# Optimization experiments

Measured on AMD Instinct MI355X. Metric: run time of the kernel, lower is better.

The kernel has to match this reference:

```python
import jax, jax.numpy as jnp
import numpy as np

B, T, D = 2, 2048, 2048
H, KV = 32, 8
HD = D // H            # 64
N_REP = H // KV        # 4


def setup_inputs() -> dict:
    key = jax.random.key(0)
    ks = jax.random.split(key, 5)
    x = jax.random.normal(ks[0], (B, T, D), dtype=jnp.float32)
    # RoPE frequencies: angle[t, i] = t / 10000^(2i/HD), i in [0, HD/2)
    inv_freq = 1.0 / (10000.0 ** (jnp.arange(0, HD, 2, dtype=jnp.float32) / HD))
    ang = jnp.arange(T, dtype=jnp.float32)[:, None] * inv_freq[None, :]  # [T, HD/2]
    freqs_cos = jnp.cos(ang)
    freqs_sin = jnp.sin(ang)
    # causal additive mask [1,1,T,T]
    r = jnp.arange(T)
    mask = jnp.where(r[None, :] > r[:, None], -1e9, 0.0).astype(jnp.float32)[None, None]
    s = 0.02
    wq = jax.random.normal(ks[1], (D, H * HD), dtype=jnp.float32) * s
    wk = jax.random.normal(ks[2], (D, KV * HD), dtype=jnp.float32) * s
    wv = jax.random.normal(ks[3], (D, KV * HD), dtype=jnp.float32) * s
    wo = jax.random.normal(ks[4], (H * HD, D), dtype=jnp.float32) * s
    return {"x": x, "freqs_cos": freqs_cos, "freqs_sin": freqs_sin, "mask": mask,
            "wq": wq, "wk": wk, "wv": wv, "wo": wo}


def _rope(t, cos, sin):
    # t: [B, T, h, HD]; complex rotation on consecutive (even, odd) pairs
    t2 = t.reshape(*t.shape[:-1], HD // 2, 2)
    c = cos[None, :, None, :]
    s = sin[None, :, None, :]
    o0 = t2[..., 0] * c - t2[..., 1] * s
    o1 = t2[..., 0] * s + t2[..., 1] * c
    return jnp.stack([o0, o1], axis=-1).reshape(t.shape)


def reference(x, freqs_cos, freqs_sin, mask, wq, wk, wv, wo):
    q = (x @ wq).reshape(B, T, H, HD)
    k = (x @ wk).reshape(B, T, KV, HD)
    v = (x @ wv).reshape(B, T, KV, HD)
    q = _rope(q, freqs_cos, freqs_sin)
    k = _rope(k, freqs_cos, freqs_sin)
    # GQA expand: each kv head repeated N_REP times consecutively
    k = jnp.repeat(k, N_REP, axis=2)  # [B, T, H, HD]
    v = jnp.repeat(v, N_REP, axis=2)
    scores = jnp.einsum('bqhd,bkhd->bhqk', q, k) / jnp.sqrt(jnp.float32(HD))
    scores = scores + mask
    attn = jax.nn.softmax(scores, axis=-1)
    out = jnp.einsum('bhqk,bkhd->bqhd', attn, v).reshape(B, T, H * HD)
    return out @ wo
```

## Files before the change

### kernel.cpp

```cpp
#include <hip/hip_runtime.h>
#include <hip/hip_bf16.h>

#define T_SEQ 2048
#define NROWS 4096
#define QKS   2560

typedef __attribute__((ext_vector_type(8))) short short8;
typedef __attribute__((ext_vector_type(4))) float f32x4;
typedef __attribute__((ext_vector_type(16))) float f32x16;
typedef __attribute__((ext_vector_type(2))) int i32x2;
typedef __attribute__((ext_vector_type(2))) unsigned int u32x2;

#define KC 0.18033688f

__device__ __forceinline__ unsigned short f2bf(float f) {
    unsigned u = __builtin_bit_cast(unsigned, f);
    u += 0x7FFF + ((u >> 16) & 1);
    return (unsigned short)(u >> 16);
}
__device__ __forceinline__ float bf2f(unsigned short s) {
    unsigned u = ((unsigned)s) << 16;
    return __builtin_bit_cast(float, u);
}

__device__ __forceinline__ void gload_lds16(const void* g, void* l) {
    __builtin_amdgcn_global_load_lds(
        (const __attribute__((address_space(1))) unsigned int*)g,
        (__attribute__((address_space(3))) unsigned int*)l,
        16, 0, 0);
}

__device__ __forceinline__ f32x4 mfma16(short8 a, short8 b, f32x4 c) {
    return __builtin_amdgcn_mfma_f32_16x16x32_bf16(a, b, c, 0, 0, 0);
}
__device__ __forceinline__ f32x16 mfma32(short8 a, short8 b, f32x16 c) {
    return __builtin_amdgcn_mfma_f32_32x32x16_bf16(a, b, c, 0, 0, 0);
}

__device__ __forceinline__ unsigned cvtpk_bf16(float lo, float hi) {
    unsigned r;
    asm("v_cvt_pk_bf16_f32 %0, %1, %2" : "=v"(r) : "v"(lo), "v"(hi));
    return r;
}

__device__ __forceinline__ short8 frag_from_u32(unsigned w0, unsigned w1, unsigned w2, unsigned w3) {
    union { unsigned u[4]; short8 s; } t;
    t.u[0] = w0; t.u[1] = w1; t.u[2] = w2; t.u[3] = w3;
    return t.s;
}

__global__ __launch_bounds__(256) void prep(const float* __restrict__ x,
                                            const float* __restrict__ wq,
                                            const float* __restrict__ wk,
                                            const float* __restrict__ wv,
                                            short* __restrict__ xb,
                                            short* __restrict__ wT) {
    __shared__ float tile[32][33];
    const int bid = blockIdx.x, t = threadIdx.x;
    if (bid < 4096) {
        const int i = bid * 256 + t;
        const float4 a = ((const float4*)x)[i * 2];
        const float4 b = ((const float4*)x)[i * 2 + 1];
        ((short8*)xb)[i] = frag_from_u32(cvtpk_bf16(a.x, a.y), cvtpk_bf16(a.z, a.w),
                                         cvtpk_bf16(b.x, b.y), cvtpk_bf16(b.z, b.w));
        return;
    }
    const int r = bid - 4096;
    const int bx = r % 96, by = r / 96;
    const float* S; int srcN, nt, dstRow0;
    if (bx < 64)      { S = wq; srcN = 2048; nt = bx;      dstRow0 = 0;    }
    else if (bx < 80) { S = wk; srcN = 512;  nt = bx - 64; dstRow0 = 2048; }
    else              { S = wv; srcN = 512;  nt = bx - 80; dstRow0 = 2560; }
    const int n0 = nt * 32, k0 = by * 32;
#pragma unroll
    for (int j = 0; j < 4; ++j) {
        int lin = t + 256 * j;
        int kk = lin >> 5, nn = lin & 31;
        tile[kk][nn] = S[(size_t)(k0 + kk) * srcN + n0 + nn];
    }
    __syncthreads();
#pragma unroll
    for (int j = 0; j < 4; ++j) {
        int lin = t + 256 * j;
        int nn = lin >> 5, kk = lin & 31;
        wT[(size_t)(dstRow0 + n0 + nn) * 2048 + k0 + kk] = (short)f2bf(tile[kk][nn]);
    }
}

__global__ __launch_bounds__(256) void transpose_f32_bf16(const float* __restrict__ S,
                                                          short* __restrict__ D,
                                                          int K, int N) {
    __shared__ float tile[32][33];
    const int n0 = blockIdx.x * 32, k0 = blockIdx.y * 32;
    const int t = threadIdx.x;
#pragma unroll
    for (int j = 0; j < 4; ++j) {
        int lin = t + 256 * j;
        int kk = lin >> 5, nn = lin & 31;
        tile[kk][nn] = S[(size_t)(k0 + kk) * N + n0 + nn];
    }
    __syncthreads();
#pragma unroll
    for (int j = 0; j < 4; ++j) {
        int lin = t + 256 * j;
        int nn = lin >> 5, kk = lin & 31;
        D[(size_t)(n0 + nn) * K + k0 + kk] = (short)f2bf(tile[kk][nn]);
    }
}

__global__ __launch_bounds__(256) void rope_vt(unsigned short* __restrict__ qk,
                                               const float* __restrict__ cosp,
                                               const float* __restrict__ sinp,
                                               const short* __restrict__ vbuf,
                                               short* __restrict__ vt) {
    __shared__ short tile[32][33];
    const int bid = blockIdx.x, t = threadIdx.x;
    if (bid < 2048) {
        const int c0 = (bid & 15) * 32, r0 = (bid >> 4) * 32;
#pragma unroll
        for (int j = 0; j < 4; ++j) {
            int lin = t + 256 * j;
            int rr = lin >> 5, cc = lin & 31;
            tile[rr][cc] = vbuf[(size_t)(r0 + rr) * 512 + c0 + cc];
        }
        __syncthreads();
#pragma unroll
        for (int j = 0; j < 4; ++j) {
            int lin = t + 256 * j;
            int cc = lin >> 5, rr = lin & 31;
            vt[(size_t)(c0 + cc) * NROWS + r0 + rr] = tile[rr][cc];
        }
        return;
    }
    int i = (bid - 2048) * 256 + t;
    int Hn = 32, c0 = 0;
    if (i >= 2097152) { i -= 2097152; Hn = 8; c0 = 2048; }
    const int gp = i * 2;
    const int p = gp & 31;
    const int hh = (gp >> 5) % Hn;
    const int row = gp / (32 * Hn);
    const int tpos = row & (T_SEQ - 1);
    const float2 cw = *(const float2*)(cosp + tpos * 32 + p);
    const float2 sw = *(const float2*)(sinp + tpos * 32 + p);
    const size_t base = (size_t)row * QKS + c0 + hh * 64 + 2 * p;
    u32x2 v = *(u32x2*)(qk + base);
    const float e0 = bf2f((unsigned short)(v.x & 0xFFFF)), o0 = bf2f((unsigned short)(v.x >> 16));
    const float e1 = bf2f((unsigned short)(v.y & 0xFFFF)), o1 = bf2f((unsigned short)(v.y >> 16));
    v.x = cvtpk_bf16(e0 * cw.x - o0 * sw.x, e0 * sw.x + o0 * cw.x);
    v.y = cvtpk_bf16(e1 * cw.y - o1 * sw.y, e1 * sw.y + o1 * cw.y);
    *(u32x2*)(qk + base) = v;
}

template <int STORE_F32>
__global__ __launch_bounds__(256) void gemm_mfma(const short* __restrict__ A,
                                                 const short* __restrict__ Bt,
                                                 void* __restrict__ C, int ldc,
                                                 short* __restrict__ Cv, int nsplit,
                                                 int M, int N, int K) {
    __shared__ short As[2][128 * 32];
    __shared__ short Bs[2][128 * 32];
    const int tid = threadIdx.x;
    const int l = tid & 63, w = tid >> 6;
    const int wr = w >> 1, wc = w & 1;
    const int lm = l & 15, lg = l >> 4;

    const int nwg = gridDim.x * gridDim.y;
    int bid = blockIdx.y * gridDim.x + blockIdx.x;
    bid = (bid & 7) * (nwg >> 3) + (bid >> 3);
    const int row0 = (bid / gridDim.x) * 128;
    const int col0 = (bid % gridDim.x) * 128;

    f32x4 acc[4][4];
#pragma unroll
    for (int m = 0; m < 4; ++m)
#pragma unroll
        for (int n = 0; n < 4; ++n) acc[m][n] = (f32x4){0.f, 0.f, 0.f, 0.f};

    auto STAGE = [&](int buf, int kt) {
        const int k0 = kt * 32;
#pragma unroll
        for (int p = 0; p < 2; ++p) {
            const int c = tid + 256 * p;
            const int r = c >> 2, k8 = (c & 3) * 8;
            gload_lds16(A  + (size_t)(row0 + r) * K + k0 + k8, &As[buf][c * 8]);
            gload_lds16(Bt + (size_t)(col0 + r) * K + k0 + k8, &Bs[buf][c * 8]);
        }
    };

    const int nk = K >> 5;
    STAGE(0, 0);
    asm volatile("s_waitcnt vmcnt(0)" ::: "memory");
    __syncthreads();

    for (int kt = 0; kt < nk; ++kt) {
        const int cur = kt & 1;
        if (kt + 1 < nk) STAGE(cur ^ 1, kt + 1);

        short8 af[4], bfr[4];
#pragma unroll
        for (int m = 0; m < 4; ++m)
            af[m] = *(const short8*)(&As[cur][(wr * 64 + m * 16 + lm) * 32 + lg * 8]);
#pragma unroll
        for (int n = 0; n < 4; ++n)
            bfr[n] = *(const short8*)(&Bs[cur][(wc * 64 + n * 16 + lm) * 32 + lg * 8]);
#pragma unroll
        for (int m = 0; m < 4; ++m)
#pragma unroll
            for (int n = 0; n < 4; ++n)
                acc[m][n] = mfma16(af[m], bfr[n], acc[m][n]);

        asm volatile("s_waitcnt vmcnt(0)" ::: "memory");
        __syncthreads();
    }

    const bool vreg = (!STORE_F32) && (col0 >= nsplit);
#pragma unroll
    for (int m = 0; m < 4; ++m)
#pragma unroll
        for (int n = 0; n < 4; ++n) {
            if (vreg) {
#pragma unroll
                for (int r = 0; r < 4; ++r) {
                    const int row = row0 + wr * 64 + m * 16 + lg * 4 + r;
                    const int col = col0 + wc * 64 + n * 16 + lm - nsplit;
                    Cv[(size_t)row * 512 + col] = (short)f2bf(acc[m][n][r]);
                }
            } else {
#pragma unroll
                for (int r = 0; r < 4; ++r) {
                    const int row = row0 + wr * 64 + m * 16 + lg * 4 + r;
                    const int col = col0 + wc * 64 + n * 16 + lm;
                    const float v = acc[m][n][r];
                    if (STORE_F32) ((float*)C)[(size_t)row * ldc + col] = v;
                    else ((unsigned short*)C)[(size_t)row * ldc + col] = f2bf(v);
                }
            }
        }
}

__global__ __launch_bounds__(256, 4) void attn_fwd(const short* __restrict__ qkv,
                                                   const short* __restrict__ vt,
                                                   unsigned short* __restrict__ aout) {
    __shared__ short Ks[2][64 * 64];
    __shared__ short Vs[2][64 * 64];
    const int bid = blockIdx.x;
    const int q2 = (bid & 3) ^ ((bid >> 8) & 3);
    const int t  = (bid >> 2) & 15;
    const int gb = ((bid >> 6) & 3) | (((bid >> 8) & 3) << 2);
    const int qt = (q2 == 0) ? t : (q2 == 1) ? (31 - t) : (q2 == 2) ? (32 + t) : (63 - t);
    const int g = gb & 7, b = gb >> 3;

    const int tid = threadIdx.x, l = tid & 63, w = tid >> 6;
    const int n = l & 31, hi = l >> 5;
    const int h = g * 4 + w;
    const int Q0 = qt * 32;
    const int qg = Q0 + n;

    const size_t krow_base = (size_t)(b * T_SEQ) * QKS + 2048 + g * 64;
    const size_t vrow_base = (size_t)(g * 64) * NROWS + b * T_SEQ;

    short8 qb[4];
    {
        const size_t qbase = (size_t)(b * T_SEQ + qg) * QKS + h * 64 + hi * 8;
        qb[0] = *(const short8*)(qkv + qbase);
        qb[1] = *(const short8*)(qkv + qbase + 16);
        qb[2] = *(const short8*)(qkv + qbase + 32);
        qb[3] = *(const short8*)(qkv + qbase + 48);
    }

    f32x16 acc0 = {}, acc1 = {};
    float m_run = -1e30f, l_run = 0.f;

    const int ntiles = (qt >> 1) + 1;

    auto STAGE = [&](int buf, int kt) {
        const int krow0 = kt * 64;
#pragma unroll
        for (int p = 0; p < 2; ++p) {
            const int c = p * 256 + tid;
            const int r = c >> 3, gk = c & 7;
            const int gs = gk ^ (r & 7);
            gload_lds16(qkv + krow_base + (size_t)(krow0 + r) * QKS + gs * 8,
                        &Ks[buf][c * 8]);
            gload_lds16(vt + vrow_base + (size_t)r * NROWS + krow0 + gs * 8,
                        &Vs[buf][c * 8]);
        }
    };

    STAGE(0, 0);
    asm volatile("s_waitcnt vmcnt(0)" ::: "memory");
    __syncthreads();

    for (int kt = 0; kt < ntiles; ++kt) {
        const int cur = kt & 1;
        if (kt + 1 < ntiles) STAGE(cur ^ 1, kt + 1);

        const int krow0 = kt * 64;
        const short* KsB = &Ks[cur][0];
        const short* VsB = &Vs[cur][0];

        f32x16 s0 = {}, s1 = {};
        __builtin_amdgcn_s_setprio(1);
#pragma unroll
        for (int ks = 0; ks < 4; ++ks) {
            const int perm = ((2 * ks + hi) ^ (n & 7)) * 8;
            const short8 kf0 = *(const short8*)(KsB + n * 64 + perm);
            const short8 kf1 = *(const short8*)(KsB + (32 + n) * 64 + perm);
            s0 = mfma32(kf0, qb[ks], s0);
            s1 = mfma32(kf1, qb[ks], s1);
        }
        __builtin_amdgcn_s_setprio(0);

        if (krow0 + 63 > Q0) {
#pragma unroll
            for (int r = 0; r < 16; ++r) {
                const int jj = krow0 + (r & 3) + 8 * (r >> 2) + 4 * hi;
                if (jj > qg) s0[r] = -1e30f;
                if (jj + 32 > qg) s1[r] = -1e30f;
            }
        }

        float t8[8];
#pragma unroll
        for (int r = 0; r < 8; ++r)
            t8[r] = fmaxf(fmaxf(s0[r], s0[r + 8]), fmaxf(s1[r], s1[r + 8]));
        float mx = fmaxf(fmaxf(fmaxf(t8[0], t8[1]), fmaxf(t8[2], t8[3])),
                         fmaxf(fmaxf(t8[4], t8[5]), fmaxf(t8[6], t8[7])));
        mx = fmaxf(mx, __shfl_xor(mx, 32));
        const float pm = mx * KC;

        if (!__all(pm <= m_run + 8.0f)) {
            const float mn = fmaxf(m_run, pm);
            const float sc = __builtin_amdgcn_exp2f(m_run - mn);
            l_run *= sc;
#pragma unroll
            for (int r = 0; r < 16; ++r) { acc0[r] *= sc; acc1[r] *= sc; }
            m_run = mn;
        }

        float ps[4] = {0.f, 0.f, 0.f, 0.f};
#pragma unroll
        for (int r = 0; r < 16; ++r) {
            const float p = __builtin_amdgcn_exp2f(__builtin_fmaf(s0[r], KC, -m_run));
            s0[r] = p; ps[r & 3] += p;
        }
#pragma unroll
        for (int r = 0; r < 16; ++r) {
            const float p = __builtin_amdgcn_exp2f(__builtin_fmaf(s1[r], KC, -m_run));
            s1[r] = p; ps[r & 3] += p;
        }
        float pst = (ps[0] + ps[1]) + (ps[2] + ps[3]);
        pst += __shfl_xor(pst, 32);
        l_run += pst;

        __builtin_amdgcn_s_setprio(1);
#define PV_STEP(KS, SV)                                                              \
        {                                                                            \
            const unsigned c01 = cvtpk_bf16(SV[((KS)&1)*8+0], SV[((KS)&1)*8+1]);     \
            const unsigned c23 = cvtpk_bf16(SV[((KS)&1)*8+2], SV[((KS)&1)*8+3]);     \
            const unsigned c45 = cvtpk_bf16(SV[((KS)&1)*8+4], SV[((KS)&1)*8+5]);     \
            const unsigned c67 = cvtpk_bf16(SV[((KS)&1)*8+6], SV[((KS)&1)*8+7]);     \
            const i32x2 r02 = __builtin_amdgcn_permlane32_swap((int)c01, (int)c45, false, false); \
            const i32x2 r13 = __builtin_amdgcn_permlane32_swap((int)c23, (int)c67, false, false); \
            const short8 pfrag = frag_from_u32((unsigned)r02.x, (unsigned)r13.x,     \
                                               (unsigned)r02.y, (unsigned)r13.y);    \
            const int permv = ((2 * (KS) + hi) ^ (n & 7)) * 8;                       \
            const short8 vf0 = *(const short8*)(VsB + n * 64 + permv);               \
            const short8 vf1 = *(const short8*)(VsB + (32 + n) * 64 + permv);        \
            acc0 = mfma32(vf0, pfrag, acc0);                                         \
            acc1 = mfma32(vf1, pfrag, acc1);                                         \
        }
        PV_STEP(0, s0)
        PV_STEP(1, s0)
        PV_STEP(2, s1)
        PV_STEP(3, s1)
#undef PV_STEP
        __builtin_amdgcn_s_setprio(0);

        asm volatile("s_waitcnt vmcnt(0)" ::: "memory");
        __syncthreads();
    }

    const float invl = 1.0f / l_run;
    const size_t orow = (size_t)(b * T_SEQ + qg) * 2048 + h * 64;
#pragma unroll
    for (int rg = 0; rg < 4; ++rg) {
        u32x2 pk0, pk1;
        pk0.x = cvtpk_bf16(acc0[rg * 4 + 0] * invl, acc0[rg * 4 + 1] * invl);
        pk0.y = cvtpk_bf16(acc0[rg * 4 + 2] * invl, acc0[rg * 4 + 3] * invl);
        pk1.x = cvtpk_bf16(acc1[rg * 4 + 0] * invl, acc1[rg * 4 + 1] * invl);
        pk1.y = cvtpk_bf16(acc1[rg * 4 + 2] * invl, acc1[rg * 4 + 3] * invl);
        *(u32x2*)(aout + orow + rg * 8 + hi * 4) = pk0;
        *(u32x2*)(aout + orow + 32 + rg * 8 + hi * 4) = pk1;
    }
}

extern "C" void kernel_launch(void* const* d_in, const int* in_sizes, int n_in,
                              void* d_out, int out_size, void* d_ws, size_t ws_size,
                              hipStream_t stream) {
    const float* x    = (const float*)d_in[0];
    const float* fcos = (const float*)d_in[1];
    const float* fsin = (const float*)d_in[2];
    const float* wq   = (const float*)d_in[4];
    const float* wk   = (const float*)d_in[5];
    const float* wv   = (const float*)d_in[6];
    const float* wo   = (const float*)d_in[7];

    short* ws0  = (short*)d_ws;
    short* qkvb = ws0;
    short* vt   = ws0 + 10485760;
    short* wT   = ws0 + 12582912;
    short* vbuf = ws0 + 18874368;
    short* aout = ws0 + 12582912;
    short* woT  = ws0;
    short* xb   = (short*)d_out;

    prep<<<10240, 256, 0, stream>>>(x, wq, wk, wv, xb, wT);
    gemm_mfma<0><<<dim3(24, 32), 256, 0, stream>>>(xb, wT, qkvb, QKS, vbuf, 2560,
                                                   NROWS, 3072, 2048);
    rope_vt<<<12288, 256, 0, stream>>>((unsigned short*)qkvb, fcos, fsin, vbuf, vt);
    attn_fwd<<<1024, 256, 0, stream>>>(qkvb, vt, (unsigned short*)aout);
    transpose_f32_bf16<<<dim3(64, 64), 256, 0, stream>>>(wo, woT, 2048, 2048);
    gemm_mfma<1><<<dim3(16, 32), 256, 0, stream>>>(aout, woT, d_out, 2048, nullptr, 1 << 30,
                                                   NROWS, 2048, 2048);
}
```

Before: 209.6 us.

## Replace 128x128 GEMM with 256x256 eight-wave tiled GEMM with swizzled LDS

The GEMM kernel moves from a 128x128 tile with 4 waves to a 256x256 tile with 8 waves per block. Each K step of 64 is split into halves, and global-to-LDS loads are interleaved between MFMA phases using fine-grained barriers, partial vmcnt waits and s_setprio. An XOR swizzle on the LDS layout is meant to avoid bank conflicts. The larger tile raises operand reuse and cuts global traffic, but the grids shrink to 192 and 128 blocks. On a 256-CU MI355X that leaves many CUs idle, and register pressure goes up.

```diff
diff --git a/kernel.cpp b/kernel.cpp
--- a/kernel.cpp
+++ b/kernel.cpp
@@ -152,84 +152,135 @@
 }
 
 template <int STORE_F32>
-__global__ __launch_bounds__(256) void gemm_mfma(const short* __restrict__ A,
-                                                 const short* __restrict__ Bt,
-                                                 void* __restrict__ C, int ldc,
-                                                 short* __restrict__ Cv, int nsplit,
-                                                 int M, int N, int K) {
-    __shared__ short As[2][128 * 32];
-    __shared__ short Bs[2][128 * 32];
+__global__ __launch_bounds__(512, 2) void gemm8(const short* __restrict__ A,
+                                                const short* __restrict__ Bt,
+                                                void* __restrict__ C, int ldc,
+                                                short* __restrict__ Cv, int nsplit,
+                                                int M, int N, int K) {
+    __shared__ short As[2][2][256 * 32];
+    __shared__ short Bs[2][2][256 * 32];
     const int tid = threadIdx.x;
     const int l = tid & 63, w = tid >> 6;
-    const int wr = w >> 1, wc = w & 1;
+    const int wm = w >> 2, wn = w & 3;
     const int lm = l & 15, lg = l >> 4;
 
     const int nwg = gridDim.x * gridDim.y;
     int bid = blockIdx.y * gridDim.x + blockIdx.x;
     bid = (bid & 7) * (nwg >> 3) + (bid >> 3);
-    const int row0 = (bid / gridDim.x) * 128;
-    const int col0 = (bid % gridDim.x) * 128;
-
-    f32x4 acc[4][4];
-#pragma unroll
-    for (int m = 0; m < 4; ++m)
+    const int row0 = (bid / gridDim.x) * 256;
+    const int col0 = (bid % gridDim.x) * 256;
+
+    const short* Abase = A + (size_t)row0 * K;
+    const short* Bbase = Bt + (size_t)col0 * K;
+
+    f32x4 acc[8][4];
+#pragma unroll
+    for (int m = 0; m < 8; ++m)
 #pragma unroll
         for (int n = 0; n < 4; ++n) acc[m][n] = (f32x4){0.f, 0.f, 0.f, 0.f};
 
-    auto STAGE = [&](int buf, int kt) {
-        const int k0 = kt * 32;
+    auto STAGEH = [&](short* dst, const short* srcbase, int kt, int kh) {
 #pragma unroll
         for (int p = 0; p < 2; ++p) {
-            const int c = tid + 256 * p;
-            const int r = c >> 2, k8 = (c & 3) * 8;
-            gload_lds16(A  + (size_t)(row0 + r) * K + k0 + k8, &As[buf][c * 8]);
-            gload_lds16(Bt + (size_t)(col0 + r) * K + k0 + k8, &Bs[buf][c * 8]);
+            const int cl = tid + 512 * p;
+            const int r = cl >> 2, gp = cl & 3;
+            const int gs = gp ^ (r & 3);
+            gload_lds16(srcbase + (size_t)r * K + kt * 64 + kh * 32 + gs * 8,
+                        dst + cl * 8);
         }
     };
 
-    const int nk = K >> 5;
-    STAGE(0, 0);
-    asm volatile("s_waitcnt vmcnt(0)" ::: "memory");
-    __syncthreads();
+#define READ_A(BUFP, MH, A4)                                                \
+    {                                                                       \
+        _Pragma("unroll")                                                   \
+        for (int i = 0; i < 4; ++i) {                                       \
+            const int r = wm * 128 + ((MH) * 4 + i) * 16 + lm;              \
+            A4[i] = *(const short8*)((BUFP) + r * 32 + (lg ^ (r & 3)) * 8); \
+        }                                                                   \
+    }
+#define READ_B(BUFP, B4)                                                    \
+    {                                                                       \
+        _Pragma("unroll")                                                   \
+        for (int i = 0; i < 4; ++i) {                                       \
+            const int r = wn * 64 + i * 16 + lm;                            \
+            B4[i] = *(const short8*)((BUFP) + r * 32 + (lg ^ (r & 3)) * 8); \
+        }                                                                   \
+    }
+#define MM16(A4, B4, MH)                                                    \
+    {                                                                       \
+        __builtin_amdgcn_s_setprio(1);                                      \
+        _Pragma("unroll")                                                   \
+        for (int i = 0; i < 4; ++i)                                         \
+            _Pragma("unroll")                                               \
+            for (int n = 0; n < 4; ++n)                                     \
+                acc[(MH) * 4 + i][n] = mfma16(A4[i], B4[n], acc[(MH) * 4 + i][n]); \
+        __builtin_amdgcn_s_setprio(0);                                      \
+    }
+
+    const int nk = K >> 6;
+    STAGEH(&As[0][0][0], Abase, 0, 0);
+    STAGEH(&Bs[0][0][0], Bbase, 0, 0);
+    STAGEH(&As[0][1][0], Abase, 0, 1);
+    STAGEH(&Bs[0][1][0], Bbase, 0, 1);
+    asm volatile("s_waitcnt vmcnt(4)" ::: "memory");
+    __builtin_amdgcn_s_barrier();
 
     for (int kt = 0; kt < nk; ++kt) {
-        const int cur = kt & 1;
-        if (kt + 1 < nk) STAGE(cur ^ 1, kt + 1);
-
-        short8 af[4], bfr[4];
-#pragma unroll
-        for (int m = 0; m < 4; ++m)
-            af[m] = *(const short8*)(&As[cur][(wr * 64 + m * 16 + lm) * 32 + lg * 8]);
-#pragma unroll
-        for (int n = 0; n < 4; ++n)
-            bfr[n] = *(const short8*)(&Bs[cur][(wc * 64 + n * 16 + lm) * 32 + lg * 8]);
-#pragma unroll
-        for (int m = 0; m < 4; ++m)
-#pragma unroll
-            for (int n = 0; n < 4; ++n)
-                acc[m][n] = mfma16(af[m], bfr[n], acc[m][n]);
-
-        asm volatile("s_waitcnt vmcnt(0)" ::: "memory");
-        __syncthreads();
-    }
+        const int buf = kt & 1, nb = buf ^ 1;
+        const bool more = (kt + 1 < nk);
+        short8 a4[4], b4[4];
+
+        READ_A(&As[buf][0][0], 0, a4);
+        READ_B(&Bs[buf][0][0], b4);
+        if (more) STAGEH(&As[nb][0][0], Abase, kt + 1, 0);
+        __builtin_amdgcn_s_barrier();
+        MM16(a4, b4, 0);
+        __builtin_amdgcn_s_barrier();
+
+        READ_A(&As[buf][0][0], 1, a4);
+        if (more) STAGEH(&Bs[nb][0][0], Bbase, kt + 1, 0);
+        __builtin_amdgcn_s_barrier();
+        MM16(a4, b4, 1);
+        if (more) asm volatile("s_waitcnt vmcnt(4)" ::: "memory");
+        else      asm volatile("s_waitcnt vmcnt(0)" ::: "memory");
+        __builtin_amdgcn_s_barrier();
+
+        READ_A(&As[buf][1][0], 0, a4);
+        READ_B(&Bs[buf][1][0], b4);
+        if (more) STAGEH(&As[nb][1][0], Abase, kt + 1, 1);
+        __builtin_amdgcn_s_barrier();
+        MM16(a4, b4, 0);
+        __builtin_amdgcn_s_barrier();
+
+        READ_A(&As[buf][1][0], 1, a4);
+        if (more) STAGEH(&Bs[nb][1][0], Bbase, kt + 1, 1);
+        __builtin_amdgcn_s_barrier();
+        MM16(a4, b4, 1);
+        if (more) asm volatile("s_waitcnt vmcnt(4)" ::: "memory");
+        else      asm volatile("s_waitcnt vmcnt(0)" ::: "memory");
+        __builtin_amdgcn_s_barrier();
+    }
+#undef READ_A
+#undef READ_B
+#undef MM16
 
     const bool vreg = (!STORE_F32) && (col0 >= nsplit);
 #pragma unroll
-    for (int m = 0; m < 4; ++m)
+    for (int m = 0; m < 8; ++m)
 #pragma unroll
         for (int n = 0; n < 4; ++n) {
             if (vreg) {
 #pragma unroll
                 for (int r = 0; r < 4; ++r) {
-                    const int row = row0 + wr * 64 + m * 16 + lg * 4 + r;
-                    const int col = col0 + wc * 64 + n * 16 + lm - nsplit;
+                    const int row = row0 + wm * 128 + m * 16 + lg * 4 + r;
+                    const int col = col0 + wn * 64 + n * 16 + lm - nsplit;
                     Cv[(size_t)row * 512 + col] = (short)f2bf(acc[m][n][r]);
                 }
             } else {
 #pragma unroll
                 for (int r = 0; r < 4; ++r) {
-                    const int row = row0 + wr * 64 + m * 16 + lg * 4 + r;
-                    const int col = col0 + wc * 64 + n * 16 + lm;
+                    const int row = row0 + wm * 128 + m * 16 + lg * 4 + r;
+                    const int col = col0 + wn * 64 + n * 16 + lm;
                     const float v = acc[m][n][r];
                     if (STORE_F32) ((float*)C)[(size_t)row * ldc + col] = v;
                     else ((unsigned short*)C)[(size_t)row * ldc + col] = f2bf(v);
@@ -416,11 +467,11 @@
     short* xb   = (short*)d_out;
 
     prep<<<10240, 256, 0, stream>>>(x, wq, wk, wv, xb, wT);
-    gemm_mfma<0><<<dim3(24, 32), 256, 0, stream>>>(xb, wT, qkvb, QKS, vbuf, 2560,
-                                                   NROWS, 3072, 2048);
+    gemm8<0><<<dim3(12, 16), 512, 0, stream>>>(xb, wT, qkvb, QKS, vbuf, 2560,
+                                               NROWS, 3072, 2048);
     rope_vt<<<12288, 256, 0, stream>>>((unsigned short*)qkvb, fcos, fsin, vbuf, vt);
     attn_fwd<<<1024, 256, 0, stream>>>(qkvb, vt, (unsigned short*)aout);
     transpose_f32_bf16<<<dim3(64, 64), 256, 0, stream>>>(wo, woT, 2048, 2048);
-    gemm_mfma<1><<<dim3(16, 32), 256, 0, stream>>>(aout, woT, d_out, 2048, nullptr, 1 << 30,
-                                                   NROWS, 2048, 2048);
-}
+    gemm8<1><<<dim3(8, 16), 512, 0, stream>>>(aout, woT, d_out, 2048, nullptr, 1 << 30,
+                                              NROWS, 2048, 2048);
+}
```

New measurement: 224.3 us. +7.0%, slower.
